# Kernel optimization log

Hardware: AMD Instinct MI355X
Metric: run time of the kernel (lower is better)

## Reference

```python
import jax, jax.numpy as jnp
import numpy as np

D, L, C, H, W = 4, 16, 64, 128, 128


def setup_inputs() -> dict:
    key = jax.random.key(0)
    ks = jax.random.split(key, 20)
    rn = lambda k, shape, s=0.02: jax.random.normal(k, shape, dtype=jnp.float32) * s
    return {
        "x": jax.random.normal(ks[0], (L, C, H, W), dtype=jnp.float32),
        "ln1_g": jnp.ones((D, C, H, W), jnp.float32),
        "ln1_b": jnp.zeros((D, C, H, W), jnp.float32),
        "Wq": rn(ks[1], (D, C, C)), "bq": jnp.zeros((D, C), jnp.float32),
        "Wk": rn(ks[2], (D, C, C)), "bk": jnp.zeros((D, C), jnp.float32),
        "Wv": rn(ks[3], (D, C, C)), "bv": jnp.zeros((D, C), jnp.float32),
        "Wa": rn(ks[4], (D, 1, 2 * C, 5, 5)), "ba": jnp.zeros((D, 1), jnp.float32),
        "ln2_g": jnp.ones((D, C, H, W), jnp.float32),
        "ln2_b": jnp.zeros((D, C, H, W), jnp.float32),
        "W1": rn(ks[5], (D, 2 * C, C)), "b1": jnp.zeros((D, 2 * C), jnp.float32),
        "W2": rn(ks[6], (D, C, 2 * C)), "b2": jnp.zeros((D, C), jnp.float32),
    }


def _layernorm(x, g, b):
    # torch nn.LayerNorm([C,H,W]): normalize over last 3 dims per frame, eps=1e-5
    mu = jnp.mean(x, axis=(1, 2, 3), keepdims=True)
    var = jnp.var(x, axis=(1, 2, 3), keepdims=True)
    return (x - mu) * jax.lax.rsqrt(var + 1e-5) * g[None] + b[None]


def _conv5(x, w):
    # x: [L, Cin, H, W], w: [1, Cin, 5, 5] -> [L, 1, H, W], SAME padding (pad=2)
    return jax.lax.conv_general_dilated(
        x, w, window_strides=(1, 1), padding="SAME",
        dimension_numbers=("NCHW", "OIHW", "NCHW"))


def _conv1x1(x, w, b):
    # 1x1 conv == per-pixel linear over channels
    return jnp.einsum("lchw,oc->lohw", x, w) + b[None, :, None, None]


def reference(x, ln1_g, ln1_b, Wq, bq, Wk, bk, Wv, bv, Wa, ba,
              ln2_g, ln2_b, W1, b1, W2, b2):
    depth = ln1_g.shape[0]
    c = Wa.shape[2] // 2
    for d in range(depth):
        # --- pre-norm conv attention (nheads=1) + residual ---
        h = _layernorm(x, ln1_g[d], ln1_b[d])
        Q = _conv1x1(h, Wq[d], bq[d])
        K = _conv1x1(h, Wk[d], bk[d])
        V = _conv1x1(h, Wv[d], bv[d])
        # conv_atten(cat([Q_i, K_j])) is linear in channels: split the 5x5
        # kernel into Q-part and K-part, so H_ij = A_i + B_j + bias.
        A = _conv5(Q, Wa[d, :, :c])[:, 0]   # [L, H, W]
        B = _conv5(K, Wa[d, :, c:])[:, 0]   # [L, H, W]
        S = A[:, None] + B[None, :] + ba[d][0]      # [L, L, H, W]
        P = jax.nn.softmax(S, axis=1)               # softmax over source frames j
        attn = jnp.einsum("ijhw,jchw->ichw", P, V)  # weighted sum of V_j
        x = x + attn
        # --- pre-norm conv FFN + residual ---
        h = _layernorm(x, ln2_g[d], ln2_b[d])
        f = _conv1x1(h, W1[d], b1[d])
        f = jax.nn.leaky_relu(f, 0.01)  # torch LeakyReLU default slope
        f = _conv1x1(f, W2[d], b2[d])
        x = x + f
    return x
```

## Files before the change

kernel.cpp:

```cpp
#include <hip/hip_runtime.h>


#define HW 16384
#define CHW 1048576
#define NB 64

typedef unsigned short u16;
typedef __attribute__((ext_vector_type(8))) _Float16 f16x8;
typedef __attribute__((ext_vector_type(8))) unsigned short u16x8;
typedef __attribute__((ext_vector_type(4))) float f32x4;

static __device__ __forceinline__ u16 f2h(float f) {
  union { _Float16 h; u16 u; } v;
  v.h = (_Float16)f;
  return v.u;
}
static __device__ __forceinline__ float h2f(u16 u) {
  union { u16 u; _Float16 h; } v;
  v.u = u;
  return (float)v.h;
}
static __device__ __forceinline__ void ln_from_acc_wave(
    const float* acc, int l, int lane, float& mu, float& r) {
  const float invN = 1.f / 1048576.f;
  float2 v = *(const float2*)(acc + lane * 32 + 2 * l);
  float s = v.x, q = v.y;
#pragma unroll
  for (int off = 32; off > 0; off >>= 1) {
    s += __shfl_xor(s, off);
    q += __shfl_xor(q, off);
  }
  mu = s * invN;
  r = rsqrtf(q * invN - mu * mu + 1e-5f);
}

__global__ __launch_bounds__(256) void prep_kernel(
    const float* __restrict__ Wa, const float* __restrict__ Wk,
    const float* __restrict__ Wv, const float* __restrict__ W1,
    const float* __restrict__ W2, u16* __restrict__ w1pk,
    u16* __restrict__ w2pk, u16* __restrict__ wvpk, u16* __restrict__ wepk) {
  int d = blockIdx.x;
  int t = blockIdx.y * 256 + threadIdx.x;
  const int STR = 256 * 16;
  const float* WaK = Wa + ((size_t)d * 128 + 64) * 25;
  const float* Wkd = Wk + d * 4096;
  for (int idx = t; idx < 2048; idx += STR) {
    int frag = idx >> 9, lane = (idx >> 3) & 63, j = idx & 7;
    int mt = frag >> 1, kt = frag & 1;
    int tap = mt * 16 + (lane & 15);
    int ci = kt * 32 + (lane >> 4) * 8 + j;
    float s = 0.f;
    if (tap < 25)
      for (int co = 0; co < 64; ++co)
        s = fmaf(WaK[co * 25 + tap], Wkd[co * 64 + ci], s);
    wepk[d * 2048 + idx] = f2h(s);
  }
  const float* Wvd = Wv + d * 4096;
  for (int idx = t; idx < 4096; idx += STR) {
    int frag = idx >> 9, lane = (idx >> 3) & 63, j = idx & 7;
    int mt = frag >> 1, kt = frag & 1;
    int co = mt * 16 + (lane & 15);
    int ci = kt * 32 + (lane >> 4) * 8 + j;
    wvpk[d * 4096 + idx] = f2h(Wvd[co * 64 + ci]);
  }
  const float* W1d = W1 + d * 8192;
  for (int idx = t; idx < 8192; idx += STR) {
    int frag = idx >> 9, lane = (idx >> 3) & 63, j = idx & 7;
    int mt = frag >> 1, kt = frag & 1;
    int o = mt * 16 + (lane & 15);
    int ci = kt * 32 + (lane >> 4) * 8 + j;
    w1pk[d * 8192 + idx] = f2h(W1d[o * 64 + ci]);
  }
  const float* W2d = W2 + d * 8192;
  for (int idx = t; idx < 8192; idx += STR) {
    int frag = idx >> 9, lane = (idx >> 3) & 63, j = idx & 7;
    int mt2 = frag >> 2, kt2 = frag & 3;
    int c = mt2 * 16 + (lane & 15);
    int o = kt2 * 32 + (lane >> 4) * 8 + j;
    w2pk[d * 8192 + idx] = f2h(W2d[c * 128 + o]);
  }
}

__global__ __launch_bounds__(256) void lngb_kernel(
    const float* __restrict__ g1, const float* __restrict__ b1,
    u16* __restrict__ o1, u16* __restrict__ o2) {
  int idx = blockIdx.x * 256 + threadIdx.x;
  const float* src = blockIdx.y == 0 ? g1 : b1;
  u16* dst = blockIdx.y == 0 ? o1 : o2;
  float4 v = *(const float4*)(src + (size_t)idx * 4);
  ushort4 o;
  o.x = f2h(v.x); o.y = f2h(v.y); o.z = f2h(v.z); o.w = f2h(v.w);
  *(ushort4*)(dst + (size_t)idx * 4) = o;
}

__global__ __launch_bounds__(256) void stats_kernel(
    const float* __restrict__ xin, u16* __restrict__ xh,
    float* __restrict__ acc) {
  int tid = threadIdx.x;
  size_t base = (size_t)blockIdx.x * 4096;
  const float4* in4 = (const float4*)(xin + base);
  float s = 0.f, q = 0.f;
#pragma unroll
  for (int k = 0; k < 4; ++k) {
    float4 v = in4[k * 256 + tid];
    ushort4 o;
    o.x = f2h(v.x); o.y = f2h(v.y); o.z = f2h(v.z); o.w = f2h(v.w);
    *(ushort4*)(xh + base + (k * 256 + tid) * 4) = o;
    s += v.x + v.y + v.z + v.w;
    q = fmaf(v.x, v.x, q); q = fmaf(v.y, v.y, q);
    q = fmaf(v.z, v.z, q); q = fmaf(v.w, v.w, q);
  }
#pragma unroll
  for (int off = 32; off > 0; off >>= 1) {
    s += __shfl_down(s, off); q += __shfl_down(q, off);
  }
  __shared__ float ls[4], lq[4];
  int wave = tid >> 6;
  if ((tid & 63) == 0) { ls[wave] = s; lq[wave] = q; }
  __syncthreads();
  if (tid == 0) {
    int frame = blockIdx.x >> 8;
    int bkt = blockIdx.x & (NB - 1);
    atomicAdd(&acc[bkt * 32 + frame * 2], ls[0] + ls[1] + ls[2] + ls[3]);
    atomicAdd(&acc[bkt * 32 + frame * 2 + 1], lq[0] + lq[1] + lq[2] + lq[3]);
  }
}

__global__ __launch_bounds__(256) void tb_kernel(
    const u16* __restrict__ xh, const u16* __restrict__ g,
    const u16* __restrict__ bln, const u16* __restrict__ wep_g,
    const float* __restrict__ accA, float* __restrict__ accBz,
    float* __restrict__ mulr, u16* __restrict__ T) {
  __shared__ __align__(16) char lds[24832];
  u16* hb = (u16*)lds;
  u16* Tb = (u16*)(lds + 18432);
  int tid = threadIdx.x;
  int l = blockIdx.y;
  int p0 = blockIdx.x << 7;
  if (blockIdx.x == 0 && blockIdx.y == 0)
    for (int i = tid; i < NB * 32; i += 256) accBz[i] = 0.f;
  int lane = tid & 63;
  float mu, r;
  ln_from_acc_wave(accA, l, lane, mu, r);
  if (blockIdx.x == 0 && tid == 0) {
    mulr[2 * l] = mu;
    mulr[2 * l + 1] = r;
  }

  {
    int pq = tid & 15, cg = tid >> 4;
    int px0 = pq * 8, c0 = cg * 4;
    float vv[4][8];
#pragma unroll
    for (int i = 0; i < 4; ++i) {
      int c = c0 + i;
      size_t gi = (((size_t)l * 64 + c) << 14) + p0 + px0;
      int li = (c << 14) + p0 + px0;
      u16x8 xv = *(const u16x8*)(xh + gi);
      u16x8 gv = *(const u16x8*)(g + li);
      u16x8 b8 = *(const u16x8*)(bln + li);
#pragma unroll
      for (int k = 0; k < 8; ++k)
        vv[i][k] = (h2f(xv[k]) - mu) * r * h2f(gv[k]) + h2f(b8[k]);
    }
#pragma unroll
    for (int k = 0; k < 8; ++k) {
      int row = px0 + k;
      int col = ((((c0 >> 3) + (row >> 2)) & 7) << 3) | (c0 & 7);
      ushort4 hv;
      hv.x = f2h(vv[0][k]); hv.y = f2h(vv[1][k]);
      hv.z = f2h(vv[2][k]); hv.w = f2h(vv[3][k]);
      *(ushort4*)(hb + row * 72 + col) = hv;
    }
  }
  __syncthreads();

  int wv = tid >> 6;
  int ln15 = lane & 15, quad = lane >> 4;

  f16x8 ah[2][2];
#pragma unroll
  for (int mt = 0; mt < 2; ++mt) {
    int px = (wv * 2 + mt) * 16 + ln15;
#pragma unroll
    for (int kt = 0; kt < 2; ++kt) {
      int slot = ((kt * 4 + quad) + (px >> 2)) & 7;
      ah[mt][kt] = *(const f16x8*)(hb + px * 72 + (slot << 3));
    }
  }
  const f16x8* weg = (const f16x8*)wep_g;

  f32x4 accT[2][2];
#pragma unroll
  for (int mt = 0; mt < 2; ++mt)
#pragma unroll
    for (int nt = 0; nt < 2; ++nt) accT[mt][nt] = (f32x4){0.f, 0.f, 0.f, 0.f};
#pragma unroll
  for (int nt = 0; nt < 2; ++nt) {
    f16x8 b0 = weg[(nt * 2 + 0) * 64 + lane];
    f16x8 b1w = weg[(nt * 2 + 1) * 64 + lane];
#pragma unroll
    for (int mt = 0; mt < 2; ++mt) {
      accT[mt][nt] = __builtin_amdgcn_mfma_f32_16x16x32_f16(
          ah[mt][0], b0, accT[mt][nt], 0, 0, 0);
      accT[mt][nt] = __builtin_amdgcn_mfma_f32_16x16x32_f16(
          ah[mt][1], b1w, accT[mt][nt], 0, 0, 0);
    }
  }

#pragma unroll
  for (int mt = 0; mt < 2; ++mt) {
    int pxl = (wv * 2 + mt) * 16 + quad * 4;
#pragma unroll
    for (int nt = 0; nt < 2; ++nt) {
      int tap = nt * 16 + ln15;
      if (tap < 25) {
        ushort4 o;
        o.x = f2h(accT[mt][nt][0]); o.y = f2h(accT[mt][nt][1]);
        o.z = f2h(accT[mt][nt][2]); o.w = f2h(accT[mt][nt][3]);
        int addr = tap * 128 + ((((pxl >> 3) + tap) & 15) << 3) + (pxl & 7);
        *(ushort4*)(Tb + addr) = o;
      }
    }
  }
  __syncthreads();
  for (int idx = tid; idx < 400; idx += 256) {
    int tap = idx >> 4, k = idx & 15;
    u16x8 v = *(const u16x8*)(Tb + tap * 128 + (((k + tap) & 15) << 3));
    *(u16x8*)(T + (((size_t)l * 25 + tap) << 14) + p0 + k * 8) = v;
  }
}

__global__ __launch_bounds__(256) void attnc_kernel(
    const u16* __restrict__ xh, const u16* __restrict__ T,
    const u16* __restrict__ g1, const u16* __restrict__ b1g,
    const u16* __restrict__ wvp_g, const float* __restrict__ bv,
    const float* __restrict__ mulr, u16* __restrict__ abf,
    float* __restrict__ accB, float* __restrict__ accAz) {
  __shared__ float Bsm[16][68];
  __shared__ float Prl[16][64];
  __shared__ float scal[64];
  __shared__ __align__(16) u16 hb[64 * 72];
  __shared__ float lsq[4][32];
  int tid = threadIdx.x;
  int p0 = blockIdx.x << 6;
  if (blockIdx.x == 0)
    for (int i = tid; i < NB * 32; i += 256) accAz[i] = 0.f;

  {
    int j = tid >> 4, xg = tid & 15;
    int y0 = p0 >> 7, x0 = p0 & 127;
    float acc4[4] = {0.f, 0.f, 0.f, 0.f};
    const u16* Tj = T + (((size_t)j * 25) << 14);
#pragma unroll
    for (int dy = 0; dy < 5; ++dy) {
      int yy = y0 + dy - 2;
      if (yy < 0 || yy > 127) continue;
#pragma unroll
      for (int dx = 0; dx < 5; ++dx) {
        const u16* Tt = Tj + ((dy * 5 + dx) << 14) + (yy << 7);
#pragma unroll
        for (int k = 0; k < 4; ++k) {
          int xc = x0 + xg * 4 + k + dx - 2;
          if (xc >= 0 && xc < 128) acc4[k] += h2f(Tt[xc]);
        }
      }
    }
#pragma unroll
    for (int k = 0; k < 4; ++k) Bsm[j][xg * 4 + k] = acc4[k];
  }
  __syncthreads();

  if (tid < 64) {
    float bj[16], m = -1e30f;
#pragma unroll
    for (int j = 0; j < 16; ++j) {
      bj[j] = Bsm[j][tid];
      m = fmaxf(m, bj[j]);
    }
    float sum = 0.f;
#pragma unroll
    for (int j = 0; j < 16; ++j) {
      bj[j] = __expf(bj[j] - m);
      sum += bj[j];
    }
    float inv = 1.f / sum;
    float sc = 0.f;
#pragma unroll
    for (int j = 0; j < 16; ++j) {
      float mu_j = mulr[2 * j], r_j = mulr[2 * j + 1];
      float prl = bj[j] * inv * r_j;
      Prl[j][tid] = prl;
      sc = fmaf(prl, mu_j, sc);
    }
    scal[tid] = sc;
  }
  __syncthreads();

  {
    int c2 = tid >> 3, pxg = tid & 7;
    int px0 = pxg * 8;
    float xbar[2][8];
#pragma unroll
    for (int cc = 0; cc < 2; ++cc)
#pragma unroll
      for (int k = 0; k < 8; ++k) xbar[cc][k] = 0.f;
#pragma unroll
    for (int j = 0; j < 16; ++j) {
      float p8[8];
#pragma unroll
      for (int k = 0; k < 8; ++k) p8[k] = Prl[j][px0 + k];
#pragma unroll
      for (int cc = 0; cc < 2; ++cc) {
        int c = cc * 32 + c2;
        u16x8 xv =
            *(const u16x8*)(xh + (((size_t)j * 64 + c) << 14) + p0 + px0);
#pragma unroll
        for (int k = 0; k < 8; ++k)
          xbar[cc][k] = fmaf(p8[k], h2f(xv[k]), xbar[cc][k]);
      }
    }
    float sc8[8];
#pragma unroll
    for (int k = 0; k < 8; ++k) sc8[k] = scal[px0 + k];
#pragma unroll
    for (int cc = 0; cc < 2; ++cc) {
      int c = cc * 32 + c2;
      int li = (c << 14) + p0 + px0;
      u16x8 g8 = *(const u16x8*)(g1 + li);
      u16x8 b8 = *(const u16x8*)(b1g + li);
#pragma unroll
      for (int k = 0; k < 8; ++k) {
        float hv = h2f(g8[k]) * (xbar[cc][k] - sc8[k]) + h2f(b8[k]);
        int row = px0 + k;
        int col = ((((c >> 3) + (row >> 2)) & 7) << 3) | (c & 7);
        hb[row * 72 + col] = f2h(hv);
      }
    }
  }
  __syncthreads();

  int wv = tid >> 6, lane = tid & 63;
  int ln15 = lane & 15, quad = lane >> 4;
  int px = wv * 16 + ln15;
  f16x8 ah[2];
#pragma unroll
  for (int kt = 0; kt < 2; ++kt) {
    int slot = ((kt * 4 + quad) + (px >> 2)) & 7;
    ah[kt] = *(const f16x8*)(hb + px * 72 + (slot << 3));
  }
  const f16x8* wvg = (const f16x8*)wvp_g;
  f32x4 accV[4];
#pragma unroll
  for (int nt = 0; nt < 4; ++nt) accV[nt] = (f32x4){0.f, 0.f, 0.f, 0.f};
#pragma unroll
  for (int nt = 0; nt < 4; ++nt) {
    f16x8 b0 = wvg[(nt * 2 + 0) * 64 + lane];
    f16x8 b1w = wvg[(nt * 2 + 1) * 64 + lane];
    accV[nt] = __builtin_amdgcn_mfma_f32_16x16x32_f16(ah[0], b0, accV[nt],
                                                      0, 0, 0);
    accV[nt] = __builtin_amdgcn_mfma_f32_16x16x32_f16(ah[1], b1w, accV[nt],
                                                      0, 0, 0);
  }
  int pxb = p0 + wv * 16 + quad * 4;
  float av[4][4];
#pragma unroll
  for (int nt = 0; nt < 4; ++nt) {
    int c = nt * 16 + ln15;
    float bvc = bv[c];
    ushort4 o;
    av[nt][0] = accV[nt][0] + bvc; o.x = f2h(av[nt][0]);
    av[nt][1] = accV[nt][1] + bvc; o.y = f2h(av[nt][1]);
    av[nt][2] = accV[nt][2] + bvc; o.z = f2h(av[nt][2]);
    av[nt][3] = accV[nt][3] + bvc; o.w = f2h(av[nt][3]);
    *(ushort4*)(abf + ((size_t)c << 14) + pxb) = o;
  }

  float sf[16], qf[16];
#pragma unroll
  for (int f = 0; f < 16; ++f) {
    float s = 0.f, q = 0.f;
#pragma unroll
    for (int nt = 0; nt < 4; ++nt) {
      int c = nt * 16 + ln15;
      ushort4 xv = *(const ushort4*)(xh + (((size_t)f * 64 + c) << 14) + pxb);
      float v0 = h2f(xv.x) + av[nt][0], v1 = h2f(xv.y) + av[nt][1];
      float v2 = h2f(xv.z) + av[nt][2], v3 = h2f(xv.w) + av[nt][3];
      s += v0 + v1 + v2 + v3;
      q = fmaf(v0, v0, q); q = fmaf(v1, v1, q);
      q = fmaf(v2, v2, q); q = fmaf(v3, v3, q);
    }
    sf[f] = s; qf[f] = q;
  }
#pragma unroll
  for (int off = 32; off > 0; off >>= 1) {
#pragma unroll
    for (int f = 0; f < 16; ++f) {
      sf[f] += __shfl_down(sf[f], off);
      qf[f] += __shfl_down(qf[f], off);
    }
  }
  if (lane == 0) {
#pragma unroll
    for (int f = 0; f < 16; ++f) {
      lsq[wv][2 * f] = sf[f];
      lsq[wv][2 * f + 1] = qf[f];
    }
  }
  __syncthreads();
  if (tid < 32) {
    int bkt = blockIdx.x & (NB - 1);
    atomicAdd(&accB[bkt * 32 + tid],
              lsq[0][tid] + lsq[1][tid] + lsq[2][tid] + lsq[3][tid]);
  }
}

__global__ __launch_bounds__(256) void ffn_kernel(
    u16* __restrict__ xh, float* __restrict__ xout,
    const u16* __restrict__ ap, const float* __restrict__ g,
    const float* __restrict__ bln, const u16* __restrict__ w1p_g,
    const float* __restrict__ b1, const u16* __restrict__ w2p_g,
    const float* __restrict__ b2, const float* __restrict__ accB,
    float* __restrict__ accA, int last) {
  __shared__ __align__(16) char lds[66560];
  float* xaf = (float*)lds;
  u16* hb = (u16*)(lds + 33792);
  u16* f1 = (u16*)(lds + 33792);

  int tid = threadIdx.x;
  int P0 = blockIdx.x << 7;
  int l = P0 >> 14;
  int p0 = P0 & 16383;
  int lane = tid & 63;
  float mu, r;
  ln_from_acc_wave(accB, l, lane, mu, r);

#pragma unroll
  for (int it = 0; it < 2; ++it) {
    int pq = tid & 31, cg = (tid >> 5) + it * 8;
    int px = pq * 4, c0 = cg * 4;
    float vv[4][4];
#pragma unroll
    for (int i = 0; i < 4; ++i) {
      int c = c0 + i;
      size_t gi = (((size_t)l * 64 + c) << 14) + p0 + px;
      int li = (c << 14) + p0 + px;
      ushort4 xv = *(const ushort4*)(xh + gi);
      ushort4 av4 = *(const ushort4*)(ap + li);
      float4 gv = *(const float4*)(g + li);
      float4 bb = *(const float4*)(bln + li);
      float4 s4;
      s4.x = h2f(xv.x) + h2f(av4.x);
      s4.y = h2f(xv.y) + h2f(av4.y);
      s4.z = h2f(xv.z) + h2f(av4.z);
      s4.w = h2f(xv.w) + h2f(av4.w);
      *(float4*)(xaf + c * 132 + px) = s4;
      vv[i][0] = (s4.x - mu) * r * gv.x + bb.x;
      vv[i][1] = (s4.y - mu) * r * gv.y + bb.y;
      vv[i][2] = (s4.z - mu) * r * gv.z + bb.z;
      vv[i][3] = (s4.w - mu) * r * gv.w + bb.w;
    }
#pragma unroll
    for (int k = 0; k < 4; ++k) {
      int row = px + k;
      int col = ((((c0 >> 3) + (row >> 2)) & 7) << 3) | (c0 & 7);
      ushort4 hv;
      hv.x = f2h(vv[0][k]); hv.y = f2h(vv[1][k]);
      hv.z = f2h(vv[2][k]); hv.w = f2h(vv[3][k]);
      *(ushort4*)(hb + row * 72 + col) = hv;
    }
  }
  __syncthreads();

  int wv = tid >> 6;
  int ln15 = lane & 15, quad = lane >> 4;

  f16x8 bh[2][2];
#pragma unroll
  for (int nt = 0; nt < 2; ++nt) {
    int px = (wv * 2 + nt) * 16 + ln15;
#pragma unroll
    for (int kt = 0; kt < 2; ++kt) {
      int slot = ((kt * 4 + quad) + (px >> 2)) & 7;
      bh[nt][kt] = *(const f16x8*)(hb + px * 72 + (slot << 3));
    }
  }
  __syncthreads();

  const f16x8* w1g = (const f16x8*)w1p_g;
  const f16x8* w2g = (const f16x8*)w2p_g;

#pragma unroll
  for (int mt = 0; mt < 8; ++mt) {
    f16x8 a1a = w1g[(mt * 2 + 0) * 64 + lane];
    f16x8 a1b = w1g[(mt * 2 + 1) * 64 + lane];
    f32x4 acc[2];
    acc[0] = (f32x4){0.f, 0.f, 0.f, 0.f};
    acc[1] = (f32x4){0.f, 0.f, 0.f, 0.f};
#pragma unroll
    for (int nt = 0; nt < 2; ++nt) {
      acc[nt] = __builtin_amdgcn_mfma_f32_16x16x32_f16(a1a, bh[nt][0],
                                                       acc[nt], 0, 0, 0);
      acc[nt] = __builtin_amdgcn_mfma_f32_16x16x32_f16(a1b, bh[nt][1],
                                                       acc[nt], 0, 0, 0);
    }
    int o0 = mt * 16 + quad * 4;
    float4 b1v = *(const float4*)(b1 + o0);
#pragma unroll
    for (int nt = 0; nt < 2; ++nt) {
      int px = (wv * 2 + nt) * 16 + ln15;
      int swz = (px & 7) * 8;
      float fv[4];
#pragma unroll
      for (int rj = 0; rj < 4; ++rj) {
        float f = acc[nt][rj] + ((const float*)&b1v)[rj];
        fv[rj] = fmaxf(f, 0.01f * f);
      }
      int col = ((o0 & ~7) ^ swz) + (o0 & 7);
      ushort4 ov;
      ov.x = f2h(fv[0]); ov.y = f2h(fv[1]);
      ov.z = f2h(fv[2]); ov.w = f2h(fv[3]);
      *(ushort4*)(f1 + px * 128 + col) = ov;
    }
  }
  __syncthreads();

  f16x8 a2[2][4];
#pragma unroll
  for (int mt = 0; mt < 2; ++mt) {
    int px = (wv * 2 + mt) * 16 + ln15;
    int swz = (px & 7) * 8;
#pragma unroll
    for (int kt = 0; kt < 4; ++kt)
      a2[mt][kt] =
          *(const f16x8*)(f1 + px * 128 + ((kt * 32 + quad * 8) ^ swz));
  }
  f32x4 acc2[2][4];
#pragma unroll
  for (int mt = 0; mt < 2; ++mt)
#pragma unroll
    for (int nt = 0; nt < 4; ++nt) acc2[mt][nt] = (f32x4){0.f, 0.f, 0.f, 0.f};
#pragma unroll
  for (int nt = 0; nt < 4; ++nt) {
    f16x8 bw[4];
#pragma unroll
    for (int kt = 0; kt < 4; ++kt) bw[kt] = w2g[(nt * 4 + kt) * 64 + lane];
#pragma unroll
    for (int mt = 0; mt < 2; ++mt)
#pragma unroll
      for (int kt = 0; kt < 4; ++kt)
        acc2[mt][nt] = __builtin_amdgcn_mfma_f32_16x16x32_f16(
            a2[mt][kt], bw[kt], acc2[mt][nt], 0, 0, 0);
  }

  float s = 0.f, q = 0.f;
#pragma unroll
  for (int mt = 0; mt < 2; ++mt) {
    int pxl = (wv * 2 + mt) * 16 + quad * 4;
#pragma unroll
    for (int nt = 0; nt < 4; ++nt) {
      int c = nt * 16 + ln15;
      float b2c = b2[c];
      const float* xac = xaf + c * 132 + pxl;
      float4 v;
      v.x = xac[0] + acc2[mt][nt][0] + b2c;
      v.y = xac[1] + acc2[mt][nt][1] + b2c;
      v.z = xac[2] + acc2[mt][nt][2] + b2c;
      v.w = xac[3] + acc2[mt][nt][3] + b2c;
      size_t gi = (((size_t)l * 64 + c) << 14) + p0 + pxl;
      if (last) {
        *(float4*)(xout + gi) = v;
      } else {
        ushort4 o;
        o.x = f2h(v.x); o.y = f2h(v.y); o.z = f2h(v.z); o.w = f2h(v.w);
        *(ushort4*)(xh + gi) = o;
      }
      s += v.x + v.y + v.z + v.w;
      q = fmaf(v.x, v.x, q); q = fmaf(v.y, v.y, q);
      q = fmaf(v.z, v.z, q); q = fmaf(v.w, v.w, q);
    }
  }
#pragma unroll
  for (int off = 32; off > 0; off >>= 1) {
    s += __shfl_down(s, off); q += __shfl_down(q, off);
  }
  if (lane == 0) {
    int bkt = blockIdx.x & (NB - 1);
    atomicAdd(&accA[bkt * 32 + l * 2], s);
    atomicAdd(&accA[bkt * 32 + l * 2 + 1], q);
  }
}

extern "C" void kernel_launch(void* const* d_in, const int* in_sizes, int n_in,
                              void* d_out, int out_size, void* d_ws,
                              size_t ws_size, hipStream_t stream) {
  const float* x_in = (const float*)d_in[0];
  const float* ln1_g = (const float*)d_in[1];
  const float* ln1_b = (const float*)d_in[2];
  const float* Wk = (const float*)d_in[5];
  const float* Wv = (const float*)d_in[7];
  const float* bv = (const float*)d_in[8];
  const float* Wa = (const float*)d_in[9];
  const float* ln2_g = (const float*)d_in[11];
  const float* ln2_b = (const float*)d_in[12];
  const float* W1 = (const float*)d_in[13];
  const float* b1 = (const float*)d_in[14];
  const float* W2 = (const float*)d_in[15];
  const float* b2 = (const float*)d_in[16];

  float* xout = (float*)d_out;
  char* wsb = (char*)d_ws;
  u16* xh = (u16*)wsb;
  u16* T = (u16*)(wsb + 33554432);
  u16* abf = (u16*)(wsb + 46661632);
  u16* g1b = (u16*)(wsb + 48758784);
  u16* b1b = (u16*)(wsb + 57147392);
  u16* w1pk = (u16*)(wsb + 65536000);
  u16* w2pk = (u16*)(wsb + 65601536);
  u16* wvpk = (u16*)(wsb + 65667072);
  u16* wepk = (u16*)(wsb + 65699840);
  float* mulr = (float*)(wsb + 65716224);
  float* accA = (float*)(wsb + 65716352);
  float* accB = (float*)(wsb + 65724544);

  hipMemsetAsync(accA, 0, 16384, stream);
  prep_kernel<<<dim3(4, 16), 256, 0, stream>>>(Wa, Wk, Wv, W1, W2, w1pk, w2pk,
                                               wvpk, wepk);
  lngb_kernel<<<dim3(4096, 2), 256, 0, stream>>>(ln1_g, ln1_b, g1b, b1b);
  stats_kernel<<<4096, 256, 0, stream>>>(x_in, xh, accA);

  for (int d = 0; d < 4; ++d) {
    tb_kernel<<<dim3(128, 16), 256, 0, stream>>>(
        xh, g1b + (size_t)d * CHW, b1b + (size_t)d * CHW, wepk + d * 2048,
        accA, accB, mulr, T);
    attnc_kernel<<<256, 256, 0, stream>>>(
        xh, T, g1b + (size_t)d * CHW, b1b + (size_t)d * CHW, wvpk + d * 4096,
        bv + d * 64, mulr, abf, accB, accA);
    ffn_kernel<<<2048, 256, 0, stream>>>(
        xh, xout, abf, ln2_g + (size_t)d * CHW, ln2_b + (size_t)d * CHW,
        w1pk + d * 8192, b1 + d * 128, w2pk + d * 8192, b2 + d * 64, accB,
        accA, d == 3 ? 1 : 0);
  }
}
```

Baseline: 507.2 us.

## Halve attention-combine tile to 32 pixels and double grid size

```diff
diff --git a/kernel.cpp b/kernel.cpp
--- a/kernel.cpp
+++ b/kernel.cpp
@@ -237,20 +237,21 @@
     const u16* __restrict__ wvp_g, const float* __restrict__ bv,
     const float* __restrict__ mulr, u16* __restrict__ abf,
     float* __restrict__ accB, float* __restrict__ accAz) {
-  __shared__ float Bsm[16][68];
-  __shared__ float Prl[16][64];
-  __shared__ float scal[64];
-  __shared__ __align__(16) u16 hb[64 * 72];
+  __shared__ float Bsm[16][36];
+  __shared__ float Prl[16][32];
+  __shared__ float scal[32];
+  __shared__ __align__(16) u16 hb[32 * 72];
+  __shared__ __align__(16) u16 ab_l[64 * 40];
   __shared__ float lsq[4][32];
   int tid = threadIdx.x;
-  int p0 = blockIdx.x << 6;
+  int p0 = blockIdx.x << 5;
   if (blockIdx.x == 0)
     for (int i = tid; i < NB * 32; i += 256) accAz[i] = 0.f;
 
   {
     int j = tid >> 4, xg = tid & 15;
     int y0 = p0 >> 7, x0 = p0 & 127;
-    float acc4[4] = {0.f, 0.f, 0.f, 0.f};
+    float acc2[2] = {0.f, 0.f};
     const u16* Tj = T + (((size_t)j * 25) << 14);
 #pragma unroll
     for (int dy = 0; dy < 5; ++dy) {
@@ -260,18 +261,18 @@
       for (int dx = 0; dx < 5; ++dx) {
         const u16* Tt = Tj + ((dy * 5 + dx) << 14) + (yy << 7);
 #pragma unroll
-        for (int k = 0; k < 4; ++k) {
-          int xc = x0 + xg * 4 + k + dx - 2;
-          if (xc >= 0 && xc < 128) acc4[k] += h2f(Tt[xc]);
+        for (int k = 0; k < 2; ++k) {
+          int xc = x0 + xg * 2 + k + dx - 2;
+          if (xc >= 0 && xc < 128) acc2[k] += h2f(Tt[xc]);
         }
       }
     }
-#pragma unroll
-    for (int k = 0; k < 4; ++k) Bsm[j][xg * 4 + k] = acc4[k];
-  }
-  __syncthreads();
-
-  if (tid < 64) {
+    Bsm[j][xg * 2] = acc2[0];
+    Bsm[j][xg * 2 + 1] = acc2[1];
+  }
+  __syncthreads();
+
+  if (tid < 32) {
     float bj[16], m = -1e30f;
 #pragma unroll
     for (int j = 0; j < 16; ++j) {
@@ -298,113 +299,111 @@
   __syncthreads();
 
   {
-    int c2 = tid >> 3, pxg = tid & 7;
+    int c2 = tid >> 2, pxg = tid & 3;
     int px0 = pxg * 8;
-    float xbar[2][8];
-#pragma unroll
-    for (int cc = 0; cc < 2; ++cc)
-#pragma unroll
-      for (int k = 0; k < 8; ++k) xbar[cc][k] = 0.f;
+    float xbar[8];
+#pragma unroll
+    for (int k = 0; k < 8; ++k) xbar[k] = 0.f;
 #pragma unroll
     for (int j = 0; j < 16; ++j) {
       float p8[8];
 #pragma unroll
       for (int k = 0; k < 8; ++k) p8[k] = Prl[j][px0 + k];
-#pragma unroll
-      for (int cc = 0; cc < 2; ++cc) {
-        int c = cc * 32 + c2;
-        u16x8 xv =
-            *(const u16x8*)(xh + (((size_t)j * 64 + c) << 14) + p0 + px0);
-#pragma unroll
-        for (int k = 0; k < 8; ++k)
-          xbar[cc][k] = fmaf(p8[k], h2f(xv[k]), xbar[cc][k]);
-      }
-    }
-    float sc8[8];
-#pragma unroll
-    for (int k = 0; k < 8; ++k) sc8[k] = scal[px0 + k];
-#pragma unroll
-    for (int cc = 0; cc < 2; ++cc) {
-      int c = cc * 32 + c2;
-      int li = (c << 14) + p0 + px0;
-      u16x8 g8 = *(const u16x8*)(g1 + li);
-      u16x8 b8 = *(const u16x8*)(b1g + li);
-#pragma unroll
-      for (int k = 0; k < 8; ++k) {
-        float hv = h2f(g8[k]) * (xbar[cc][k] - sc8[k]) + h2f(b8[k]);
-        int row = px0 + k;
-        int col = ((((c >> 3) + (row >> 2)) & 7) << 3) | (c & 7);
-        hb[row * 72 + col] = f2h(hv);
-      }
+      u16x8 xv =
+          *(const u16x8*)(xh + (((size_t)j * 64 + c2) << 14) + p0 + px0);
+#pragma unroll
+      for (int k = 0; k < 8; ++k)
+        xbar[k] = fmaf(p8[k], h2f(xv[k]), xbar[k]);
+    }
+    int li = (c2 << 14) + p0 + px0;
+    u16x8 g8 = *(const u16x8*)(g1 + li);
+    u16x8 b8 = *(const u16x8*)(b1g + li);
+#pragma unroll
+    for (int k = 0; k < 8; ++k) {
+      float hv = h2f(g8[k]) * (xbar[k] - scal[px0 + k]) + h2f(b8[k]);
+      int row = px0 + k;
+      int col = ((((c2 >> 3) + (row >> 2)) & 7) << 3) | (c2 & 7);
+      hb[row * 72 + col] = f2h(hv);
     }
   }
   __syncthreads();
 
   int wv = tid >> 6, lane = tid & 63;
   int ln15 = lane & 15, quad = lane >> 4;
-  int px = wv * 16 + ln15;
-  f16x8 ah[2];
-#pragma unroll
-  for (int kt = 0; kt < 2; ++kt) {
-    int slot = ((kt * 4 + quad) + (px >> 2)) & 7;
-    ah[kt] = *(const f16x8*)(hb + px * 72 + (slot << 3));
-  }
-  const f16x8* wvg = (const f16x8*)wvp_g;
-  f32x4 accV[4];
-#pragma unroll
-  for (int nt = 0; nt < 4; ++nt) accV[nt] = (f32x4){0.f, 0.f, 0.f, 0.f};
-#pragma unroll
-  for (int nt = 0; nt < 4; ++nt) {
-    f16x8 b0 = wvg[(nt * 2 + 0) * 64 + lane];
-    f16x8 b1w = wvg[(nt * 2 + 1) * 64 + lane];
-    accV[nt] = __builtin_amdgcn_mfma_f32_16x16x32_f16(ah[0], b0, accV[nt],
-                                                      0, 0, 0);
-    accV[nt] = __builtin_amdgcn_mfma_f32_16x16x32_f16(ah[1], b1w, accV[nt],
-                                                      0, 0, 0);
-  }
-  int pxb = p0 + wv * 16 + quad * 4;
-  float av[4][4];
-#pragma unroll
-  for (int nt = 0; nt < 4; ++nt) {
-    int c = nt * 16 + ln15;
-    float bvc = bv[c];
-    ushort4 o;
-    av[nt][0] = accV[nt][0] + bvc; o.x = f2h(av[nt][0]);
-    av[nt][1] = accV[nt][1] + bvc; o.y = f2h(av[nt][1]);
-    av[nt][2] = accV[nt][2] + bvc; o.z = f2h(av[nt][2]);
-    av[nt][3] = accV[nt][3] + bvc; o.w = f2h(av[nt][3]);
-    *(ushort4*)(abf + ((size_t)c << 14) + pxb) = o;
-  }
-
-  float sf[16], qf[16];
-#pragma unroll
-  for (int f = 0; f < 16; ++f) {
-    float s = 0.f, q = 0.f;
+  if (wv < 2) {
+    int px = wv * 16 + ln15;
+    f16x8 ah[2];
+#pragma unroll
+    for (int kt = 0; kt < 2; ++kt) {
+      int slot = ((kt * 4 + quad) + (px >> 2)) & 7;
+      ah[kt] = *(const f16x8*)(hb + px * 72 + (slot << 3));
+    }
+    const f16x8* wvg = (const f16x8*)wvp_g;
+    f32x4 accV[4];
+#pragma unroll
+    for (int nt = 0; nt < 4; ++nt) accV[nt] = (f32x4){0.f, 0.f, 0.f, 0.f};
+#pragma unroll
+    for (int nt = 0; nt < 4; ++nt) {
+      f16x8 b0 = wvg[(nt * 2 + 0) * 64 + lane];
+      f16x8 b1w = wvg[(nt * 2 + 1) * 64 + lane];
+      accV[nt] = __builtin_amdgcn_mfma_f32_16x16x32_f16(ah[0], b0, accV[nt],
+                                                        0, 0, 0);
+      accV[nt] = __builtin_amdgcn_mfma_f32_16x16x32_f16(ah[1], b1w, accV[nt],
+                                                        0, 0, 0);
+    }
+    int pxl = wv * 16 + quad * 4;
+    int pxb = p0 + pxl;
 #pragma unroll
     for (int nt = 0; nt < 4; ++nt) {
       int c = nt * 16 + ln15;
-      ushort4 xv = *(const ushort4*)(xh + (((size_t)f * 64 + c) << 14) + pxb);
-      float v0 = h2f(xv.x) + av[nt][0], v1 = h2f(xv.y) + av[nt][1];
-      float v2 = h2f(xv.z) + av[nt][2], v3 = h2f(xv.w) + av[nt][3];
-      s += v0 + v1 + v2 + v3;
-      q = fmaf(v0, v0, q); q = fmaf(v1, v1, q);
-      q = fmaf(v2, v2, q); q = fmaf(v3, v3, q);
-    }
-    sf[f] = s; qf[f] = q;
-  }
-#pragma unroll
-  for (int off = 32; off > 0; off >>= 1) {
+      float bvc = bv[c];
+      ushort4 o;
+      o.x = f2h(accV[nt][0] + bvc);
+      o.y = f2h(accV[nt][1] + bvc);
+      o.z = f2h(accV[nt][2] + bvc);
+      o.w = f2h(accV[nt][3] + bvc);
+      *(ushort4*)(abf + ((size_t)c << 14) + pxb) = o;
+      *(ushort4*)(ab_l + c * 40 + pxl) = o;
+    }
+  }
+  __syncthreads();
+
+  {
+    int c2 = tid >> 2, pxg = tid & 3;
+    int px0 = pxg * 8;
+    u16x8 a8 = *(const u16x8*)(ab_l + c2 * 40 + px0);
+    float af[8];
+#pragma unroll
+    for (int k = 0; k < 8; ++k) af[k] = h2f(a8[k]);
+    float sf[16], qf[16];
 #pragma unroll
     for (int f = 0; f < 16; ++f) {
-      sf[f] += __shfl_down(sf[f], off);
-      qf[f] += __shfl_down(qf[f], off);
-    }
-  }
-  if (lane == 0) {
-#pragma unroll
-    for (int f = 0; f < 16; ++f) {
-      lsq[wv][2 * f] = sf[f];
-      lsq[wv][2 * f + 1] = qf[f];
+      u16x8 xv =
+          *(const u16x8*)(xh + (((size_t)f * 64 + c2) << 14) + p0 + px0);
+      float s = 0.f, q = 0.f;
+#pragma unroll
+      for (int k = 0; k < 8; ++k) {
+        float v = h2f(xv[k]) + af[k];
+        s += v;
+        q = fmaf(v, v, q);
+      }
+      sf[f] = s;
+      qf[f] = q;
+    }
+#pragma unroll
+    for (int off = 32; off > 0; off >>= 1) {
+#pragma unroll
+      for (int f = 0; f < 16; ++f) {
+        sf[f] += __shfl_down(sf[f], off);
+        qf[f] += __shfl_down(qf[f], off);
+      }
+    }
+    if (lane == 0) {
+#pragma unroll
+      for (int f = 0; f < 16; ++f) {
+        lsq[wv][2 * f] = sf[f];
+        lsq[wv][2 * f + 1] = qf[f];
+      }
     }
   }
   __syncthreads();
@@ -633,7 +632,7 @@
     tb_kernel<<<dim3(128, 16), 256, 0, stream>>>(
         xh, g1b + (size_t)d * CHW, b1b + (size_t)d * CHW, wepk + d * 2048,
         accA, accB, mulr, T);
-    attnc_kernel<<<256, 256, 0, stream>>>(
+    attnc_kernel<<<512, 256, 0, stream>>>(
         xh, T, g1b + (size_t)d * CHW, b1b + (size_t)d * CHW, wvpk + d * 4096,
         bv + d * 64, mulr, abf, accB, accA);
     ffn_kernel<<<2048, 256, 0, stream>>>(
```

Result: slower. 532.7 us (+5.0%).
